# Kernel optimization log

Hardware: AMD Instinct MI355X
Metric: run time of the kernel (lower is better)

## Reference

```python
import jax, jax.numpy as jnp
import numpy as np
from jax import lax

DIM = 512
HEADS = 8


def _branch(x, w1, wd):
    # 1x1 pointwise conv (no bias)
    y = jnp.einsum('oc,bchw->bohw', w1, x)
    # ReflectionPad2d(2)
    y = jnp.pad(y, ((0, 0), (0, 0), (2, 2), (2, 2)), mode='reflect')
    # depthwise 3x3, dilation 2, valid padding (net: same spatial size)
    y = lax.conv_general_dilated(
        y, wd, window_strides=(1, 1), padding='VALID', rhs_dilation=(2, 2),
        dimension_numbers=('NCHW', 'OIHW', 'NCHW'), feature_group_count=y.shape[1])
    return y


def setup_inputs() -> dict:
    key = jax.random.key(0)
    ks = jax.random.split(key, 8)
    s = 0.02
    style_feat = jax.random.normal(ks[0], (16, DIM, 64, 64), dtype=jnp.float32)
    fw1 = jax.random.normal(ks[1], (DIM, DIM), dtype=jnp.float32) * s
    fwd_ = jax.random.normal(ks[2], (DIM, 1, 3, 3), dtype=jnp.float32) * s
    gw1 = jax.random.normal(ks[3], (DIM, DIM), dtype=jnp.float32) * s
    gwd = jax.random.normal(ks[4], (DIM, 1, 3, 3), dtype=jnp.float32) * s
    hw1 = jax.random.normal(ks[5], (DIM, DIM), dtype=jnp.float32) * s
    hwd = jax.random.normal(ks[6], (DIM, 1, 3, 3), dtype=jnp.float32) * s
    ow = jax.random.normal(ks[7], (DIM, DIM), dtype=jnp.float32) * s
    temperature = jnp.ones((HEADS, 1, 1), dtype=jnp.float32)
    return dict(style_feat=style_feat, fw1=fw1, fwd_=fwd_, gw1=gw1, gwd=gwd,
                hw1=hw1, hwd=hwd, ow=ow, temperature=temperature)


def reference(style_feat, fw1, fwd_, gw1, gwd, hw1, hwd, ow, temperature):
    B, C, H, W = style_feat.shape
    cph = C // HEADS
    f_x = _branch(style_feat, fw1, fwd_)
    g_x = _branch(style_feat, gw1, gwd)
    h_x = _branch(style_feat, hw1, hwd)
    q = f_x.reshape(B, HEADS, cph, H * W)
    k = g_x.reshape(B, HEADS, cph, H * W)
    v = h_x.reshape(B, HEADS, cph, H * W)
    # channel-wise attention: [B,h,cph,cph]
    energy = jnp.einsum('bhcn,bhdn->bhcd', q, k)
    attn = jax.nn.softmax(energy * temperature[None], axis=-1)
    out = jnp.einsum('bhcd,bhdn->bhcn', attn, v).reshape(B, C, H, W)
    out = jnp.einsum('oc,bchw->bohw', ow, out)
    return out + style_feat
```

## Files before the change

### kernel.cpp

```cpp
#include <hip/hip_runtime.h>

typedef unsigned short u16;
typedef __bf16 bf8_t __attribute__((ext_vector_type(8)));
typedef short short8 __attribute__((ext_vector_type(8)));
typedef float f32x4 __attribute__((ext_vector_type(4)));

#define DEV __device__ __forceinline__

DEV u16 f2bf(float x) {
  unsigned u = __builtin_bit_cast(unsigned, x);
  return (u16)((u + 0x7FFFu + ((u >> 16) & 1u)) >> 16);
}
DEV float bf2f(u16 x) {
  unsigned u = (unsigned)x << 16;
  return __builtin_bit_cast(float, u);
}

__global__ void k_wconv(const float* __restrict__ f, const float* __restrict__ g,
                        const float* __restrict__ h, u16* __restrict__ out) {
  int i = blockIdx.x * 256 + threadIdx.x;
  float v;
  if (i < 262144) v = f[i];
  else if (i < 524288) v = g[i - 262144];
  else v = h[i - 524288];
  out[i] = f2bf(v);
}

__global__ __launch_bounds__(256) void k_xt(const float* __restrict__ style, u16* __restrict__ Xt) {
  __shared__ float t[32][33];
  int b = blockIdx.z, c0 = blockIdx.y * 32, n0 = blockIdx.x * 32;
  int tid = threadIdx.x, lr = tid >> 5, lc = tid & 31;
  const float* src = style + ((size_t)b * 512 + c0) * 4096 + n0;
#pragma unroll
  for (int it = 0; it < 4; ++it) {
    int r = it * 8 + lr;
    t[r][lc] = src[(size_t)r * 4096 + lc];
  }
  __syncthreads();
  u16* dst = Xt + ((size_t)b * 4096 + n0) * 512 + c0;
#pragma unroll
  for (int it = 0; it < 4; ++it) {
    int n = it * 8 + lr;
    dst[(size_t)n * 512 + lc] = f2bf(t[lc][n]);
  }
}

DEV void gload16(const u16* g, u16* l) {
  __builtin_amdgcn_global_load_lds((__attribute__((address_space(1))) void*)(g),
                                   (__attribute__((address_space(3))) void*)(l), 16, 0, 0);
}

DEV void stage_tile(const u16* __restrict__ src, int row0, int kb,
                    u16* lds, int wave, int lane) {
#pragma unroll
  for (int qq = 0; qq < 2; ++qq) {
    int idx = (wave * 2 + qq) * 64 + lane;
    int r = idx >> 2;
    int cb = (idx & 3) * 8;
    gload16(src + (size_t)(row0 + r) * 512 + (kb + cb),
            lds + (wave * 2 + qq) * 512);
  }
}

__global__ __launch_bounds__(256, 2) void k_gemm_branch(
    const u16* __restrict__ Wbf, const u16* __restrict__ Xt, u16* __restrict__ Y) {
  int z = blockIdx.z;
  int t = z >> 4, b = z & 15;
  const u16* A = Wbf + (size_t)t * (512 * 512);
  const u16* B = Xt + (size_t)b * (4096 * 512);
  u16* C = Y + (size_t)z * (512 * 4096);
  int M0 = blockIdx.y * 128, N0 = blockIdx.x * 128;
  int tid = threadIdx.x, wave = tid >> 6, lane = tid & 63;
  int wm = wave >> 1, wn = wave & 1;
  __shared__ __align__(16) u16 lA[2][128 * 32];
  __shared__ __align__(16) u16 lB[2][128 * 32];
  f32x4 acc[4][4];
#pragma unroll
  for (int m = 0; m < 4; ++m)
#pragma unroll
    for (int n = 0; n < 4; ++n) acc[m][n] = (f32x4){0.f, 0.f, 0.f, 0.f};
  stage_tile(A, M0, 0, &lA[0][0], wave, lane);
  stage_tile(B, N0, 0, &lB[0][0], wave, lane);
  __syncthreads();
  int lrow = lane & 15, lk = (lane >> 4) * 8;
#pragma unroll 2
  for (int kt = 0; kt < 16; ++kt) {
    int cur = kt & 1;
    if (kt < 15) {
      stage_tile(A, M0, (kt + 1) * 32, &lA[cur ^ 1][0], wave, lane);
      stage_tile(B, N0, (kt + 1) * 32, &lB[cur ^ 1][0], wave, lane);
    }
    bf8_t af[4], bff[4];
#pragma unroll
    for (int m = 0; m < 4; ++m)
      af[m] = *(const bf8_t*)&lA[cur][(wm * 64 + m * 16 + lrow) * 32 + lk];
#pragma unroll
    for (int n = 0; n < 4; ++n)
      bff[n] = *(const bf8_t*)&lB[cur][(wn * 64 + n * 16 + lrow) * 32 + lk];
#pragma unroll
    for (int m = 0; m < 4; ++m)
#pragma unroll
      for (int n = 0; n < 4; ++n)
        acc[m][n] = __builtin_amdgcn_mfma_f32_16x16x32_bf16(af[m], bff[n], acc[m][n], 0, 0, 0);
    __syncthreads();
  }
  int orow = (lane >> 4) * 4, ocol = lane & 15;
#pragma unroll
  for (int m = 0; m < 4; ++m)
#pragma unroll
    for (int n = 0; n < 4; ++n) {
      int row = M0 + wm * 64 + m * 16 + orow;
      int col = N0 + wn * 64 + n * 16 + ocol;
      u16* cp = C + (size_t)row * 4096 + col;
#pragma unroll
      for (int i = 0; i < 4; ++i) cp[(size_t)i * 4096] = f2bf(acc[m][n][i]);
    }
}

__global__ __launch_bounds__(256) void k_dw(u16* __restrict__ Y,
    const float* __restrict__ fwd, const float* __restrict__ gwd, const float* __restrict__ hwd) {
  int p = blockIdx.x;
  int c = p & 511;
  int t = p >> 13;
  const float* wsrc = (t == 0) ? fwd : (t == 1) ? gwd : hwd;
  __shared__ float w[9];
  __shared__ float pl[4096];
  int tid = threadIdx.x;
  if (tid < 9) w[tid] = wsrc[c * 9 + tid];
  u16* plane = Y + (size_t)p * 4096;
#pragma unroll
  for (int qq = 0; qq < 2; ++qq) {
    int v = tid * 2 + qq;
    short8 d = *(const short8*)(plane + v * 8);
#pragma unroll
    for (int e = 0; e < 8; ++e) pl[v * 8 + e] = bf2f((u16)d[e]);
  }
  __syncthreads();
  int y = tid >> 2, xb = (tid & 3) * 16;
  float o[16];
#pragma unroll
  for (int e = 0; e < 16; ++e) o[e] = 0.f;
#pragma unroll
  for (int i = 0; i < 3; ++i) {
    int yy = y + 2 * i - 2;
    yy = yy < 0 ? -yy : (yy > 63 ? 126 - yy : yy);
    const float* row = pl + yy * 64;
#pragma unroll
    for (int j = 0; j < 3; ++j) {
      float wv = w[i * 3 + j];
#pragma unroll
      for (int e = 0; e < 16; ++e) {
        int xx = xb + e + 2 * j - 2;
        xx = xx < 0 ? -xx : (xx > 63 ? 126 - xx : xx);
        o[e] += wv * row[xx];
      }
    }
  }
  short8 s0, s1;
#pragma unroll
  for (int e = 0; e < 8; ++e) { s0[e] = (short)f2bf(o[e]); s1[e] = (short)f2bf(o[e + 8]); }
  *(short8*)(plane + y * 64 + xb) = s0;
  *(short8*)(plane + y * 64 + xb + 8) = s1;
}

__global__ __launch_bounds__(256) void k_vt(const u16* __restrict__ Y, u16* __restrict__ Vt) {
  __shared__ u16 tb[64][72];
  int b = blockIdx.z, c0 = blockIdx.y * 64, n0 = blockIdx.x * 64;
  int tid = threadIdx.x, r = tid >> 2, q = tid & 3;
  const u16* src = Y + ((size_t)(32 + b) * 512 + c0) * 4096 + n0;
  short8 d0 = *(const short8*)(src + (size_t)r * 4096 + q * 16);
  short8 d1 = *(const short8*)(src + (size_t)r * 4096 + q * 16 + 8);
#pragma unroll
  for (int e = 0; e < 8; ++e) { tb[r][q * 16 + e] = (u16)d0[e]; tb[r][q * 16 + 8 + e] = (u16)d1[e]; }
  __syncthreads();
  u16* dst = Vt + ((size_t)b * 4096 + n0) * 512 + c0;
  short8 s0, s1;
#pragma unroll
  for (int e = 0; e < 8; ++e) { s0[e] = (short)tb[q * 16 + e][r]; s1[e] = (short)tb[q * 16 + 8 + e][r]; }
  *(short8*)(dst + (size_t)r * 512 + q * 16) = s0;
  *(short8*)(dst + (size_t)r * 512 + q * 16 + 8) = s1;
}

__global__ __launch_bounds__(256) void k_energy(const u16* __restrict__ Y, float* __restrict__ E) {
  int half = blockIdx.x, h = blockIdx.y, b = blockIdx.z;
  int tid = threadIdx.x, wave = tid >> 6, lane = tid & 63;
  const u16* q = Y + ((size_t)b * 512 + h * 64) * 4096;
  const u16* k = Y + ((size_t)(16 + b) * 512 + h * 64) * 4096;
  f32x4 acc[4][4];
#pragma unroll
  for (int m = 0; m < 4; ++m)
#pragma unroll
    for (int n = 0; n < 4; ++n) acc[m][n] = (f32x4){0.f, 0.f, 0.f, 0.f};
  int lrow = lane & 15, lk = (lane >> 4) * 8;
  int nstart = half * 1024 + wave * 256;
#pragma unroll 1
  for (int it = 0; it < 8; ++it) {
    int nb = nstart + it * 32;
    bf8_t af[4], bff[4];
#pragma unroll
    for (int m = 0; m < 4; ++m)
      af[m] = *(const bf8_t*)(q + (size_t)(m * 16 + lrow) * 4096 + nb + lk);
#pragma unroll
    for (int n = 0; n < 4; ++n)
      bff[n] = *(const bf8_t*)(k + (size_t)(n * 16 + lrow) * 4096 + nb + lk);
#pragma unroll
    for (int m = 0; m < 4; ++m)
#pragma unroll
      for (int n = 0; n < 4; ++n)
        acc[m][n] = __builtin_amdgcn_mfma_f32_16x16x32_bf16(af[m], bff[n], acc[m][n], 0, 0, 0);
  }
  __shared__ float red[4][4096];
  int orow = (lane >> 4) * 4, ocol = lane & 15;
#pragma unroll
  for (int m = 0; m < 4; ++m)
#pragma unroll
    for (int n = 0; n < 4; ++n)
#pragma unroll
      for (int i = 0; i < 4; ++i)
        red[wave][(m * 16 + orow + i) * 64 + n * 16 + ocol] = acc[m][n][i];
  __syncthreads();
  float* Eo = E + ((size_t)(half * 16 + b) * 8 + h) * 4096;
  for (int v = tid; v < 4096; v += 256)
    Eo[v] = red[0][v] + red[1][v] + red[2][v] + red[3][v];
}

__global__ __launch_bounds__(64) void k_softmax(float* __restrict__ E, const float* __restrict__ temp) {
  int bh = blockIdx.x;
  int b = bh >> 3, h = bh & 7;
  int c = threadIdx.x;
  float* p0 = E + (((size_t)b * 8 + h) * 64 + c) * 64;
  float tv = temp[h];
  float e[64];
  float mx = -1e30f;
#pragma unroll
  for (int d = 0; d < 64; ++d) {
    float v = (p0[d] + p0[d + 524288] + p0[d + 1048576] + p0[d + 1572864]) * tv;
    e[d] = v;
    mx = fmaxf(mx, v);
  }
  float s = 0.f;
#pragma unroll
  for (int d = 0; d < 64; ++d) { float v = __expf(e[d] - mx); e[d] = v; s += v; }
  float inv = 1.f / s;
#pragma unroll
  for (int d = 0; d < 64; ++d) p0[d] = e[d] * inv;
}

__global__ __launch_bounds__(256) void k_m2(const float* __restrict__ E, const float* __restrict__ ow,
                                            u16* __restrict__ M2) {
  int og = blockIdx.x, h = blockIdx.y, b = blockIdx.z;
  __shared__ float at[4096];
  int tid = threadIdx.x;
  const float* attn = E + ((size_t)b * 8 + h) * 4096;
  for (int v = tid; v < 4096; v += 256) at[v] = attn[v];
  __syncthreads();
  int o = og * 64 + (tid >> 2), dq = (tid & 3) * 16;
  const float* owr = ow + (size_t)o * 512 + h * 64;
  float acc[16];
#pragma unroll
  for (int e = 0; e < 16; ++e) acc[e] = 0.f;
  for (int cc = 0; cc < 64; ++cc) {
    float wv = owr[cc];
#pragma unroll
    for (int e = 0; e < 16; ++e) acc[e] += wv * at[cc * 64 + dq + e];
  }
  u16* dst = M2 + ((size_t)b * 512 + o) * 512 + h * 64 + dq;
  short8 s0, s1;
#pragma unroll
  for (int e = 0; e < 8; ++e) { s0[e] = (short)f2bf(acc[e]); s1[e] = (short)f2bf(acc[e + 8]); }
  *(short8*)dst = s0;
  *(short8*)(dst + 8) = s1;
}

__global__ __launch_bounds__(256, 2) void k_gemm_final(
    const u16* __restrict__ M2, const u16* __restrict__ Vt,
    const float* __restrict__ style, float* __restrict__ out) {
  int b = blockIdx.z;
  const u16* A = M2 + (size_t)b * (512 * 512);
  const u16* B = Vt + (size_t)b * (4096 * 512);
  const float* st = style + (size_t)b * (512 * 4096);
  float* op = out + (size_t)b * (512 * 4096);
  int M0 = blockIdx.y * 128, N0 = blockIdx.x * 128;
  int tid = threadIdx.x, wave = tid >> 6, lane = tid & 63;
  int wm = wave >> 1, wn = wave & 1;
  __shared__ __align__(16) u16 lA[2][128 * 32];
  __shared__ __align__(16) u16 lB[2][128 * 32];
  f32x4 acc[4][4];
#pragma unroll
  for (int m = 0; m < 4; ++m)
#pragma unroll
    for (int n = 0; n < 4; ++n) acc[m][n] = (f32x4){0.f, 0.f, 0.f, 0.f};
  stage_tile(A, M0, 0, &lA[0][0], wave, lane);
  stage_tile(B, N0, 0, &lB[0][0], wave, lane);
  __syncthreads();
  int lrow = lane & 15, lk = (lane >> 4) * 8;
#pragma unroll 2
  for (int kt = 0; kt < 16; ++kt) {
    int cur = kt & 1;
    if (kt < 15) {
      stage_tile(A, M0, (kt + 1) * 32, &lA[cur ^ 1][0], wave, lane);
      stage_tile(B, N0, (kt + 1) * 32, &lB[cur ^ 1][0], wave, lane);
    }
    bf8_t af[4], bff[4];
#pragma unroll
    for (int m = 0; m < 4; ++m)
      af[m] = *(const bf8_t*)&lA[cur][(wm * 64 + m * 16 + lrow) * 32 + lk];
#pragma unroll
    for (int n = 0; n < 4; ++n)
      bff[n] = *(const bf8_t*)&lB[cur][(wn * 64 + n * 16 + lrow) * 32 + lk];
#pragma unroll
    for (int m = 0; m < 4; ++m)
#pragma unroll
      for (int n = 0; n < 4; ++n)
        acc[m][n] = __builtin_amdgcn_mfma_f32_16x16x32_bf16(af[m], bff[n], acc[m][n], 0, 0, 0);
    __syncthreads();
  }
  int orow = (lane >> 4) * 4, ocol = lane & 15;
#pragma unroll
  for (int m = 0; m < 4; ++m)
#pragma unroll
    for (int n = 0; n < 4; ++n) {
      int row = M0 + wm * 64 + m * 16 + orow;
      int col = N0 + wn * 64 + n * 16 + ocol;
      float* cp = op + (size_t)row * 4096 + col;
      const float* sp = st + (size_t)row * 4096 + col;
#pragma unroll
      for (int i = 0; i < 4; ++i) cp[(size_t)i * 4096] = acc[m][n][i] + sp[(size_t)i * 4096];
    }
}


extern "C" void kernel_launch(void* const* d_in, const int* in_sizes, int n_in,
                              void* d_out, int out_size, void* d_ws, size_t ws_size,
                              hipStream_t stream) {
  const float* style = (const float*)d_in[0];
  const float* fw1   = (const float*)d_in[1];
  const float* fwd_  = (const float*)d_in[2];
  const float* gw1   = (const float*)d_in[3];
  const float* gwd   = (const float*)d_in[4];
  const float* hw1   = (const float*)d_in[5];
  const float* hwd   = (const float*)d_in[6];
  const float* ow    = (const float*)d_in[7];
  const float* temp  = (const float*)d_in[8];
  float* out = (float*)d_out;

  char* ws = (char*)d_ws;
  u16*   Wbf = (u16*)(ws + 0);
  u16*   Y   = (u16*)(ws + (size_t)2097152);
  u16*   Xt  = (u16*)(ws + (size_t)203423744);
  u16*   Vt  = Xt;
  float* E   = (float*)(ws + (size_t)270532608);
  u16*   M2  = (u16*)(ws + (size_t)278921216);

  k_wconv<<<3072, 256, 0, stream>>>(fw1, gw1, hw1, Wbf);
  k_xt<<<dim3(128, 16, 16), 256, 0, stream>>>(style, Xt);
  k_gemm_branch<<<dim3(32, 4, 48), 256, 0, stream>>>(Wbf, Xt, Y);
  k_dw<<<24576, 256, 0, stream>>>(Y, fwd_, gwd, hwd);
  k_vt<<<dim3(64, 8, 16), 256, 0, stream>>>(Y, Vt);
  k_energy<<<dim3(4, 8, 16), 256, 0, stream>>>(Y, E);
  k_softmax<<<128, 64, 0, stream>>>(E, temp);
  k_m2<<<dim3(8, 8, 16), 256, 0, stream>>>(E, ow, M2);
  k_gemm_final<<<dim3(32, 4, 16), 256, 0, stream>>>(M2, Vt, style, out);
}
```

Measured before the change: 469.9 us.

## Replace branch GEMM with 256x256 tiled, swizzled, phased MFMA kernel fusing three weights

Replaces the 128x128 branch GEMM with a 512-thread kernel that computes 256x256 tiles over a concatenated 1536-row weight matrix. It uses XOR-swizzled LDS, K-steps of 64, and explicit vmcnt/barrier phasing with setprio around MFMA quads. The Y layout becomes per-batch [1536 rows], and the dw, vt and energy kernels are reindexed to match. The aims are more data reuse per LDS load, fewer bank conflicts, and loads overlapped with math. In exchange it uses more LDS and registers per block, and the hand-scheduled waits add complexity.

```diff
diff --git a/kernel.cpp b/kernel.cpp
--- a/kernel.cpp
+++ b/kernel.cpp
@@ -15,6 +15,16 @@
   unsigned u = (unsigned)x << 16;
   return __builtin_bit_cast(float, u);
 }
+
+DEV void gload16(const u16* g, u16* l) {
+  __builtin_amdgcn_global_load_lds((__attribute__((address_space(1))) void*)(g),
+                                   (__attribute__((address_space(3))) void*)(l), 16, 0, 0);
+}
+
+#define BARRIER() do { asm volatile("" ::: "memory"); __builtin_amdgcn_s_barrier(); asm volatile("" ::: "memory"); } while (0)
+#define VMCNT(n) asm volatile("s_waitcnt vmcnt(" #n ")" ::: "memory")
+#define PRIO1 __builtin_amdgcn_s_setprio(1)
+#define PRIO0 __builtin_amdgcn_s_setprio(0)
 
 __global__ void k_wconv(const float* __restrict__ f, const float* __restrict__ g,
                         const float* __restrict__ h, u16* __restrict__ out) {
@@ -45,9 +55,133 @@
   }
 }
 
-DEV void gload16(const u16* g, u16* l) {
-  __builtin_amdgcn_global_load_lds((__attribute__((address_space(1))) void*)(g),
-                                   (__attribute__((address_space(3))) void*)(l), 16, 0, 0);
+
+DEV void stage_half(const u16* mat, int rc0, int kt, int half,
+                    u16* ldsslot, int wave, int lane) {
+  const u16* base = mat + (size_t)(rc0 + half * 128) * 512 + kt * 64;
+  u16* ldsb = ldsslot + half * (128 * 64);
+#pragma unroll
+  for (int q = 0; q < 2; ++q) {
+    int ci = (wave * 2 + q) * 64 + lane;
+    int r = ci >> 3;
+    int scb = (ci & 7) ^ (r & 7);
+    gload16(base + (size_t)r * 512 + scb * 8, ldsb + (wave * 2 + q) * 512);
+  }
+}
+
+DEV bf8_t rdfrag(const u16* slot, int row, int ks, int lkg) {
+  int off = (ks * 64 + lkg * 16) ^ ((row & 7) << 4);
+  return *(const bf8_t*)((const char*)slot + row * 128 + off);
+}
+
+#define RD_A(dst, slot, mofs)                                     \
+  _Pragma("unroll") for (int m = 0; m < 4; ++m)                   \
+  _Pragma("unroll") for (int ks = 0; ks < 2; ++ks)                \
+    dst[m][ks] = rdfrag(slot, wm * 128 + (mofs) + m * 16 + lrow, ks, lkg);
+
+#define RD_B(dst, slot, nofs)                                     \
+  _Pragma("unroll") for (int n = 0; n < 2; ++n)                   \
+  _Pragma("unroll") for (int ks = 0; ks < 2; ++ks)                \
+    dst[n][ks] = rdfrag(slot, wn * 64 + (nofs) + n * 16 + lrow, ks, lkg);
+
+#define QUAD(AF, BF, MB, NB)                                                              \
+  do {                                                                                    \
+    _Pragma("unroll") for (int m = 0; m < 4; ++m)                                         \
+    _Pragma("unroll") for (int n = 0; n < 2; ++n) {                                       \
+      acc[(MB) + m][(NB) + n] = __builtin_amdgcn_mfma_f32_16x16x32_bf16(                  \
+          AF[m][0], BF[n][0], acc[(MB) + m][(NB) + n], 0, 0, 0);                          \
+      acc[(MB) + m][(NB) + n] = __builtin_amdgcn_mfma_f32_16x16x32_bf16(                  \
+          AF[m][1], BF[n][1], acc[(MB) + m][(NB) + n], 0, 0, 0);                          \
+    }                                                                                     \
+  } while (0)
+
+#define PHASES4(slotA, slotB, S0, S1, S2, S3, VMSTMT)   \
+  RD_A(a0, slotA, 0);                                   \
+  RD_B(b0, slotB, 0);                                   \
+  S0;                                                   \
+  BARRIER();                                            \
+  PRIO1; QUAD(a0, b0, 0, 0); PRIO0;                     \
+  BARRIER();                                            \
+  RD_A(a1, slotA, 64);                                  \
+  S1;                                                   \
+  BARRIER();                                            \
+  PRIO1; QUAD(a1, b0, 4, 0); PRIO0;                     \
+  BARRIER();                                            \
+  RD_B(b1, slotB, 32);                                  \
+  S2;                                                   \
+  BARRIER();                                            \
+  PRIO1; QUAD(a0, b1, 0, 2); PRIO0;                     \
+  BARRIER();                                            \
+  S3;                                                   \
+  BARRIER();                                            \
+  PRIO1; QUAD(a1, b1, 4, 2); PRIO0;                     \
+  VMSTMT;                                               \
+  BARRIER();
+
+__global__ __launch_bounds__(512, 2) void k_gemm256_branch(
+    const u16* __restrict__ Wall, const u16* __restrict__ Xt, u16* __restrict__ Y) {
+  int bid = blockIdx.x;
+  int wg = (bid & 7) * 192 + (bid >> 3);
+  int b = wg / 96;
+  int rr = wg % 96;
+  int nt = rr / 6, mt = rr % 6;
+  int M0 = mt * 256, N0 = nt * 256;
+  const u16* A = Wall;
+  const u16* B = Xt + (size_t)b * (4096 * 512);
+  u16* C = Y + (size_t)b * (1536 * 4096);
+
+  int tid = threadIdx.x, wave = tid >> 6, lane = tid & 63;
+  int wm = wave >> 2, wn = wave & 3;
+  int lrow = lane & 15, lkg = lane >> 4;
+
+  __shared__ __align__(16) u16 lA[2][256 * 64];
+  __shared__ __align__(16) u16 lB[2][256 * 64];
+
+  f32x4 acc[8][4];
+#pragma unroll
+  for (int m = 0; m < 8; ++m)
+#pragma unroll
+    for (int n = 0; n < 4; ++n) acc[m][n] = (f32x4){0.f, 0.f, 0.f, 0.f};
+
+  stage_half(A, M0, 0, 0, lA[0], wave, lane);
+  stage_half(A, M0, 0, 1, lA[0], wave, lane);
+  stage_half(B, N0, 0, 0, lB[0], wave, lane);
+  stage_half(B, N0, 0, 1, lB[0], wave, lane);
+  stage_half(A, M0, 1, 0, lA[1], wave, lane);
+  stage_half(A, M0, 1, 1, lA[1], wave, lane);
+  VMCNT(4);
+  BARRIER();
+
+  bf8_t a0[4][2], a1[4][2], b0[2][2], b1[2][2];
+#pragma unroll 1
+  for (int it = 0; it < 4; ++it) {
+    const int T = it * 2;
+    const bool last = (it == 3);
+    PHASES4(lA[0], lB[0],
+            stage_half(B, N0, T + 1, 0, lB[1], wave, lane),
+            stage_half(B, N0, T + 1, 1, lB[1], wave, lane),
+            if (!last) stage_half(A, M0, T + 2, 0, lA[0], wave, lane),
+            if (!last) stage_half(A, M0, T + 2, 1, lA[0], wave, lane),
+            if (last) { VMCNT(0); } else { VMCNT(4); })
+    PHASES4(lA[1], lB[1],
+            if (!last) stage_half(B, N0, T + 2, 0, lB[0], wave, lane),
+            if (!last) stage_half(B, N0, T + 2, 1, lB[0], wave, lane),
+            if (!last) stage_half(A, M0, T + 3, 0, lA[1], wave, lane),
+            if (!last) stage_half(A, M0, T + 3, 1, lA[1], wave, lane),
+            if (!last) { VMCNT(4); })
+  }
+
+  int orow = lkg * 4, ocol = lrow;
+#pragma unroll
+  for (int am = 0; am < 8; ++am)
+#pragma unroll
+    for (int an = 0; an < 4; ++an) {
+      int row = M0 + wm * 128 + am * 16 + orow;
+      int col = N0 + wn * 64 + an * 16 + ocol;
+      u16* cp = C + (size_t)row * 4096 + col;
+#pragma unroll
+      for (int i = 0; i < 4; ++i) cp[(size_t)i * 4096] = f2bf(acc[am][an][i]);
+    }
 }
 
 DEV void stage_tile(const u16* __restrict__ src, int row0, int kb,
@@ -62,66 +196,11 @@
   }
 }
 
-__global__ __launch_bounds__(256, 2) void k_gemm_branch(
-    const u16* __restrict__ Wbf, const u16* __restrict__ Xt, u16* __restrict__ Y) {
-  int z = blockIdx.z;
-  int t = z >> 4, b = z & 15;
-  const u16* A = Wbf + (size_t)t * (512 * 512);
-  const u16* B = Xt + (size_t)b * (4096 * 512);
-  u16* C = Y + (size_t)z * (512 * 4096);
-  int M0 = blockIdx.y * 128, N0 = blockIdx.x * 128;
-  int tid = threadIdx.x, wave = tid >> 6, lane = tid & 63;
-  int wm = wave >> 1, wn = wave & 1;
-  __shared__ __align__(16) u16 lA[2][128 * 32];
-  __shared__ __align__(16) u16 lB[2][128 * 32];
-  f32x4 acc[4][4];
-#pragma unroll
-  for (int m = 0; m < 4; ++m)
-#pragma unroll
-    for (int n = 0; n < 4; ++n) acc[m][n] = (f32x4){0.f, 0.f, 0.f, 0.f};
-  stage_tile(A, M0, 0, &lA[0][0], wave, lane);
-  stage_tile(B, N0, 0, &lB[0][0], wave, lane);
-  __syncthreads();
-  int lrow = lane & 15, lk = (lane >> 4) * 8;
-#pragma unroll 2
-  for (int kt = 0; kt < 16; ++kt) {
-    int cur = kt & 1;
-    if (kt < 15) {
-      stage_tile(A, M0, (kt + 1) * 32, &lA[cur ^ 1][0], wave, lane);
-      stage_tile(B, N0, (kt + 1) * 32, &lB[cur ^ 1][0], wave, lane);
-    }
-    bf8_t af[4], bff[4];
-#pragma unroll
-    for (int m = 0; m < 4; ++m)
-      af[m] = *(const bf8_t*)&lA[cur][(wm * 64 + m * 16 + lrow) * 32 + lk];
-#pragma unroll
-    for (int n = 0; n < 4; ++n)
-      bff[n] = *(const bf8_t*)&lB[cur][(wn * 64 + n * 16 + lrow) * 32 + lk];
-#pragma unroll
-    for (int m = 0; m < 4; ++m)
-#pragma unroll
-      for (int n = 0; n < 4; ++n)
-        acc[m][n] = __builtin_amdgcn_mfma_f32_16x16x32_bf16(af[m], bff[n], acc[m][n], 0, 0, 0);
-    __syncthreads();
-  }
-  int orow = (lane >> 4) * 4, ocol = lane & 15;
-#pragma unroll
-  for (int m = 0; m < 4; ++m)
-#pragma unroll
-    for (int n = 0; n < 4; ++n) {
-      int row = M0 + wm * 64 + m * 16 + orow;
-      int col = N0 + wn * 64 + n * 16 + ocol;
-      u16* cp = C + (size_t)row * 4096 + col;
-#pragma unroll
-      for (int i = 0; i < 4; ++i) cp[(size_t)i * 4096] = f2bf(acc[m][n][i]);
-    }
-}
-
 __global__ __launch_bounds__(256) void k_dw(u16* __restrict__ Y,
     const float* __restrict__ fwd, const float* __restrict__ gwd, const float* __restrict__ hwd) {
   int p = blockIdx.x;
-  int c = p & 511;
-  int t = p >> 13;
+  int within = p % 1536;
+  int t = within >> 9, c = within & 511;
   const float* wsrc = (t == 0) ? fwd : (t == 1) ? gwd : hwd;
   __shared__ float w[9];
   __shared__ float pl[4096];
@@ -167,7 +246,7 @@
   __shared__ u16 tb[64][72];
   int b = blockIdx.z, c0 = blockIdx.y * 64, n0 = blockIdx.x * 64;
   int tid = threadIdx.x, r = tid >> 2, q = tid & 3;
-  const u16* src = Y + ((size_t)(32 + b) * 512 + c0) * 4096 + n0;
+  const u16* src = Y + ((size_t)b * 1536 + 1024 + c0) * 4096 + n0;
   short8 d0 = *(const short8*)(src + (size_t)r * 4096 + q * 16);
   short8 d1 = *(const short8*)(src + (size_t)r * 4096 + q * 16 + 8);
 #pragma unroll
@@ -184,8 +263,8 @@
 __global__ __launch_bounds__(256) void k_energy(const u16* __restrict__ Y, float* __restrict__ E) {
   int half = blockIdx.x, h = blockIdx.y, b = blockIdx.z;
   int tid = threadIdx.x, wave = tid >> 6, lane = tid & 63;
-  const u16* q = Y + ((size_t)b * 512 + h * 64) * 4096;
-  const u16* k = Y + ((size_t)(16 + b) * 512 + h * 64) * 4096;
+  const u16* q = Y + ((size_t)b * 1536 + h * 64) * 4096;
+  const u16* k = Y + ((size_t)b * 1536 + 512 + h * 64) * 4096;
   f32x4 acc[4][4];
 #pragma unroll
   for (int m = 0; m < 4; ++m)
@@ -354,7 +433,7 @@
 
   k_wconv<<<3072, 256, 0, stream>>>(fw1, gw1, hw1, Wbf);
   k_xt<<<dim3(128, 16, 16), 256, 0, stream>>>(style, Xt);
-  k_gemm_branch<<<dim3(32, 4, 48), 256, 0, stream>>>(Wbf, Xt, Y);
+  k_gemm256_branch<<<1536, 512, 0, stream>>>(Wbf, Xt, Y);
   k_dw<<<24576, 256, 0, stream>>>(Y, fwd_, gwd, hwd);
   k_vt<<<dim3(64, 8, 16), 256, 0, stream>>>(Y, Vt);
   k_energy<<<dim3(4, 8, 16), 256, 0, stream>>>(Y, E);
```

Measured after the change: 478.2 us. About the same (+1.8%).

## Fuse depthwise conv into energy and V-transpose kernels, remap GEMM grid per XCD

Applied to the files above, without the earlier changes.

The branch GEMM now treats the three pointwise weights as one 1536-row matrix and uses a flat grid that assigns two batches to each XCD, so each batch's Xt stays in that XCD's L2. The separate depthwise-conv, V-transpose and energy kernels are replaced by two fused kernels. k_dwE computes the dilated 3x3 conv for q and k into swizzled LDS and feeds MFMA energy accumulation over row bands. k_dwV convolves v and writes it transposed straight to Vt. This removes an in-place rewrite of Y and a separate transpose pass over global memory, at the cost of recomputing reflection indexing in registers and lower parallelism in the fused kernels.

```diff
diff --git a/kernel.cpp b/kernel.cpp
--- a/kernel.cpp
+++ b/kernel.cpp
@@ -14,6 +14,11 @@
 DEV float bf2f(u16 x) {
   unsigned u = (unsigned)x << 16;
   return __builtin_bit_cast(float, u);
+}
+
+DEV void gload16(const u16* g, u16* l) {
+  __builtin_amdgcn_global_load_lds((__attribute__((address_space(1))) void*)(g),
+                                   (__attribute__((address_space(3))) void*)(l), 16, 0, 0);
 }
 
 __global__ void k_wconv(const float* __restrict__ f, const float* __restrict__ g,
@@ -45,11 +50,6 @@
   }
 }
 
-DEV void gload16(const u16* g, u16* l) {
-  __builtin_amdgcn_global_load_lds((__attribute__((address_space(1))) void*)(g),
-                                   (__attribute__((address_space(3))) void*)(l), 16, 0, 0);
-}
-
 DEV void stage_tile(const u16* __restrict__ src, int row0, int kb,
                     u16* lds, int wave, int lane) {
 #pragma unroll
@@ -63,13 +63,17 @@
 }
 
 __global__ __launch_bounds__(256, 2) void k_gemm_branch(
-    const u16* __restrict__ Wbf, const u16* __restrict__ Xt, u16* __restrict__ Y) {
-  int z = blockIdx.z;
-  int t = z >> 4, b = z & 15;
-  const u16* A = Wbf + (size_t)t * (512 * 512);
+    const u16* __restrict__ Wall, const u16* __restrict__ Xt, u16* __restrict__ Y) {
+  int bid = blockIdx.x;
+  int xcd = bid & 7, idx = bid >> 3;
+  int bh = idx / 384;
+  int r = idx - bh * 384;
+  int b = xcd * 2 + bh;
+  int nt = r / 12, mt = r - nt * 12;
+  int M0 = mt * 128, N0 = nt * 128;
+  const u16* A = Wall;
   const u16* B = Xt + (size_t)b * (4096 * 512);
-  u16* C = Y + (size_t)z * (512 * 4096);
-  int M0 = blockIdx.y * 128, N0 = blockIdx.x * 128;
+  u16* C = Y + (size_t)b * (1536 * 4096);
   int tid = threadIdx.x, wave = tid >> 6, lane = tid & 63;
   int wm = wave >> 1, wn = wave & 1;
   __shared__ __align__(16) u16 lA[2][128 * 32];
@@ -117,111 +121,146 @@
     }
 }
 
-__global__ __launch_bounds__(256) void k_dw(u16* __restrict__ Y,
-    const float* __restrict__ fwd, const float* __restrict__ gwd, const float* __restrict__ hwd) {
-  int p = blockIdx.x;
-  int c = p & 511;
-  int t = p >> 13;
-  const float* wsrc = (t == 0) ? fwd : (t == 1) ? gwd : hwd;
-  __shared__ float w[9];
-  __shared__ float pl[4096];
-  int tid = threadIdx.x;
-  if (tid < 9) w[tid] = wsrc[c * 9 + tid];
-  u16* plane = Y + (size_t)p * 4096;
-#pragma unroll
-  for (int qq = 0; qq < 2; ++qq) {
-    int v = tid * 2 + qq;
-    short8 d = *(const short8*)(plane + v * 8);
-#pragma unroll
-    for (int e = 0; e < 8; ++e) pl[v * 8 + e] = bf2f((u16)d[e]);
-  }
-  __syncthreads();
-  int y = tid >> 2, xb = (tid & 3) * 16;
-  float o[16];
-#pragma unroll
-  for (int e = 0; e < 16; ++e) o[e] = 0.f;
+template <typename F>
+DEV void dw_row(const u16* plane, const float* w9, int y, F&& store) {
+  short8 raw[3][8];
 #pragma unroll
   for (int i = 0; i < 3; ++i) {
     int yy = y + 2 * i - 2;
     yy = yy < 0 ? -yy : (yy > 63 ? 126 - yy : yy);
-    const float* row = pl + yy * 64;
-#pragma unroll
-    for (int j = 0; j < 3; ++j) {
-      float wv = w[i * 3 + j];
-#pragma unroll
-      for (int e = 0; e < 16; ++e) {
-        int xx = xb + e + 2 * j - 2;
-        xx = xx < 0 ? -xx : (xx > 63 ? 126 - xx : xx);
-        o[e] += wv * row[xx];
+    const short8* rp = (const short8*)(plane + yy * 64);
+#pragma unroll
+    for (int ch = 0; ch < 8; ++ch) raw[i][ch] = rp[ch];
+  }
+#pragma unroll
+  for (int g = 0; g < 4; ++g) {
+    float fr[3][20];
+#pragma unroll
+    for (int t = 0; t < 20; ++t) {
+      int p = g * 16 - 2 + t;
+      int rp2 = p < 0 ? -p : (p > 63 ? 126 - p : p);
+#pragma unroll
+      for (int i = 0; i < 3; ++i)
+        fr[i][t] = bf2f((u16)raw[i][rp2 >> 3][rp2 & 7]);
+    }
+    float o[16];
+#pragma unroll
+    for (int e = 0; e < 16; ++e) {
+      float s = 0.f;
+#pragma unroll
+      for (int i = 0; i < 3; ++i)
+#pragma unroll
+        for (int j = 0; j < 3; ++j)
+          s += w9[i * 3 + j] * fr[i][e + 2 * j];
+      o[e] = s;
+    }
+    store(g, o);
+  }
+}
+
+__global__ __launch_bounds__(256, 2) void k_dwE(const u16* __restrict__ Y,
+    const float* __restrict__ fwd, const float* __restrict__ gwd, float* __restrict__ E) {
+  int band = blockIdx.x, h = blockIdx.y, b = blockIdx.z;
+  __shared__ __align__(16) u16 qbuf[64 * 256];
+  __shared__ __align__(16) u16 kbuf[64 * 256];
+  int tid = threadIdx.x;
+  int c = ((tid >> 5) << 3) | (tid & 7);
+  int yl = (tid >> 3) & 3;
+  int wv = tid >> 6, lane = tid & 63;
+  int lrow = lane & 15, lkg = lane >> 4;
+  const u16* qp = Y + ((size_t)b * 1536 + h * 64 + c) * 4096;
+  const u16* kp = Y + ((size_t)b * 1536 + 512 + h * 64 + c) * 4096;
+  float wq9[9], wk9[9];
+#pragma unroll
+  for (int t = 0; t < 9; ++t) {
+    wq9[t] = fwd[(h * 64 + c) * 9 + t];
+    wk9[t] = gwd[(h * 64 + c) * 9 + t];
+  }
+  f32x4 acc[4];
+#pragma unroll
+  for (int n = 0; n < 4; ++n) acc[n] = (f32x4){0.f, 0.f, 0.f, 0.f};
+  char* qrow = (char*)qbuf + c * 512;
+  char* krow = (char*)kbuf + c * 512;
+  int c7 = c & 7;
+#pragma unroll 1
+  for (int sb = 0; sb < 4; ++sb) {
+    int y = band * 16 + sb * 4 + yl;
+    dw_row(qp, wq9, y, [&](int g, const float* o) {
+      short8 s0, s1;
+#pragma unroll
+      for (int e = 0; e < 8; ++e) { s0[e] = (short)f2bf(o[e]); s1[e] = (short)f2bf(o[e + 8]); }
+      int ch0 = yl * 8 + g * 2;
+      *(short8*)(qrow + 16 * (ch0 ^ c7)) = s0;
+      *(short8*)(qrow + 16 * ((ch0 + 1) ^ c7)) = s1;
+    });
+    dw_row(kp, wk9, y, [&](int g, const float* o) {
+      short8 s0, s1;
+#pragma unroll
+      for (int e = 0; e < 8; ++e) { s0[e] = (short)f2bf(o[e]); s1[e] = (short)f2bf(o[e + 8]); }
+      int ch0 = yl * 8 + g * 2;
+      *(short8*)(krow + 16 * (ch0 ^ c7)) = s0;
+      *(short8*)(krow + 16 * ((ch0 + 1) ^ c7)) = s1;
+    });
+    __syncthreads();
+    const char* qb = (const char*)qbuf + (wv * 16 + lrow) * 512;
+    int ca7 = (wv * 16 + lrow) & 7;
+#pragma unroll
+    for (int ks = 0; ks < 8; ++ks) {
+      bf8_t aF = *(const bf8_t*)(qb + 16 * ((ks * 4 + lkg) ^ ca7));
+#pragma unroll
+      for (int n = 0; n < 4; ++n) {
+        int cb = n * 16 + lrow;
+        bf8_t bF = *(const bf8_t*)((const char*)kbuf + cb * 512 + 16 * ((ks * 4 + lkg) ^ (cb & 7)));
+        acc[n] = __builtin_amdgcn_mfma_f32_16x16x32_bf16(aF, bF, acc[n], 0, 0, 0);
       }
     }
-  }
-  short8 s0, s1;
-#pragma unroll
-  for (int e = 0; e < 8; ++e) { s0[e] = (short)f2bf(o[e]); s1[e] = (short)f2bf(o[e + 8]); }
-  *(short8*)(plane + y * 64 + xb) = s0;
-  *(short8*)(plane + y * 64 + xb + 8) = s1;
-}
-
-__global__ __launch_bounds__(256) void k_vt(const u16* __restrict__ Y, u16* __restrict__ Vt) {
-  __shared__ u16 tb[64][72];
-  int b = blockIdx.z, c0 = blockIdx.y * 64, n0 = blockIdx.x * 64;
-  int tid = threadIdx.x, r = tid >> 2, q = tid & 3;
-  const u16* src = Y + ((size_t)(32 + b) * 512 + c0) * 4096 + n0;
-  short8 d0 = *(const short8*)(src + (size_t)r * 4096 + q * 16);
-  short8 d1 = *(const short8*)(src + (size_t)r * 4096 + q * 16 + 8);
-#pragma unroll
-  for (int e = 0; e < 8; ++e) { tb[r][q * 16 + e] = (u16)d0[e]; tb[r][q * 16 + 8 + e] = (u16)d1[e]; }
-  __syncthreads();
-  u16* dst = Vt + ((size_t)b * 4096 + n0) * 512 + c0;
-  short8 s0, s1;
-#pragma unroll
-  for (int e = 0; e < 8; ++e) { s0[e] = (short)tb[q * 16 + e][r]; s1[e] = (short)tb[q * 16 + 8 + e][r]; }
-  *(short8*)(dst + (size_t)r * 512 + q * 16) = s0;
-  *(short8*)(dst + (size_t)r * 512 + q * 16 + 8) = s1;
-}
-
-__global__ __launch_bounds__(256) void k_energy(const u16* __restrict__ Y, float* __restrict__ E) {
-  int half = blockIdx.x, h = blockIdx.y, b = blockIdx.z;
-  int tid = threadIdx.x, wave = tid >> 6, lane = tid & 63;
-  const u16* q = Y + ((size_t)b * 512 + h * 64) * 4096;
-  const u16* k = Y + ((size_t)(16 + b) * 512 + h * 64) * 4096;
-  f32x4 acc[4][4];
-#pragma unroll
-  for (int m = 0; m < 4; ++m)
-#pragma unroll
-    for (int n = 0; n < 4; ++n) acc[m][n] = (f32x4){0.f, 0.f, 0.f, 0.f};
-  int lrow = lane & 15, lk = (lane >> 4) * 8;
-  int nstart = half * 1024 + wave * 256;
+    __syncthreads();
+  }
+  float* Eo = E + (((size_t)band * 16 + b) * 8 + h) * 4096;
+  int orow = (lane >> 4) * 4, ocol = lane & 15;
+#pragma unroll
+  for (int n = 0; n < 4; ++n)
+#pragma unroll
+    for (int i = 0; i < 4; ++i)
+      Eo[(wv * 16 + orow + i) * 64 + n * 16 + ocol] = acc[n][i];
+}
+
+__global__ __launch_bounds__(256, 2) void k_dwV(const u16* __restrict__ Y,
+    const float* __restrict__ hwd, u16* __restrict__ Vt) {
+  int band = blockIdx.x, ct = blockIdx.y, b = blockIdx.z;
+  __shared__ float vb[256 * 68];
+  int tid = threadIdx.x;
+  int c = ((tid >> 5) << 3) | (tid & 7);
+  int yl = (tid >> 3) & 3;
+  int cg = tid & 7;
+  int cglob = ct * 64 + c;
+  const u16* plane = Y + ((size_t)b * 1536 + 1024 + cglob) * 4096;
+  float w9[9];
+#pragma unroll
+  for (int t = 0; t < 9; ++t) w9[t] = hwd[cglob * 9 + t];
 #pragma unroll 1
-  for (int it = 0; it < 8; ++it) {
-    int nb = nstart + it * 32;
-    bf8_t af[4], bff[4];
-#pragma unroll
-    for (int m = 0; m < 4; ++m)
-      af[m] = *(const bf8_t*)(q + (size_t)(m * 16 + lrow) * 4096 + nb + lk);
-#pragma unroll
-    for (int n = 0; n < 4; ++n)
-      bff[n] = *(const bf8_t*)(k + (size_t)(n * 16 + lrow) * 4096 + nb + lk);
-#pragma unroll
-    for (int m = 0; m < 4; ++m)
-#pragma unroll
-      for (int n = 0; n < 4; ++n)
-        acc[m][n] = __builtin_amdgcn_mfma_f32_16x16x32_bf16(af[m], bff[n], acc[m][n], 0, 0, 0);
-  }
-  __shared__ float red[4][4096];
-  int orow = (lane >> 4) * 4, ocol = lane & 15;
-#pragma unroll
-  for (int m = 0; m < 4; ++m)
-#pragma unroll
-    for (int n = 0; n < 4; ++n)
-#pragma unroll
-      for (int i = 0; i < 4; ++i)
-        red[wave][(m * 16 + orow + i) * 64 + n * 16 + ocol] = acc[m][n][i];
-  __syncthreads();
-  float* Eo = E + ((size_t)(half * 16 + b) * 8 + h) * 4096;
-  for (int v = tid; v < 4096; v += 256)
-    Eo[v] = red[0][v] + red[1][v] + red[2][v] + red[3][v];
+  for (int sb = 0; sb < 4; ++sb) {
+    int y = band * 16 + sb * 4 + yl;
+    dw_row(plane, w9, y, [&](int g, const float* o) {
+#pragma unroll
+      for (int e = 0; e < 16; ++e)
+        vb[((g * 16 + e) * 4 + yl) * 68 + c] = o[e];
+    });
+    __syncthreads();
+#pragma unroll
+    for (int k = 0; k < 8; ++k) {
+      int np = (tid >> 3) + 32 * k;
+      int x = np >> 2, yy = np & 3;
+      int ng = (band * 16 + sb * 4 + yy) * 64 + x;
+      f32x4 r0 = *(const f32x4*)&vb[np * 68 + cg * 8];
+      f32x4 r1 = *(const f32x4*)&vb[np * 68 + cg * 8 + 4];
+      short8 s;
+#pragma unroll
+      for (int e = 0; e < 4; ++e) { s[e] = (short)f2bf(r0[e]); s[e + 4] = (short)f2bf(r1[e]); }
+      *(short8*)(Vt + ((size_t)b * 4096 + ng) * 512 + ct * 64 + cg * 8) = s;
+    }
+    __syncthreads();
+  }
 }
 
 __global__ __launch_bounds__(64) void k_softmax(float* __restrict__ E, const float* __restrict__ temp) {
@@ -354,10 +393,9 @@
 
   k_wconv<<<3072, 256, 0, stream>>>(fw1, gw1, hw1, Wbf);
   k_xt<<<dim3(128, 16, 16), 256, 0, stream>>>(style, Xt);
-  k_gemm_branch<<<dim3(32, 4, 48), 256, 0, stream>>>(Wbf, Xt, Y);
-  k_dw<<<24576, 256, 0, stream>>>(Y, fwd_, gwd, hwd);
-  k_vt<<<dim3(64, 8, 16), 256, 0, stream>>>(Y, Vt);
-  k_energy<<<dim3(4, 8, 16), 256, 0, stream>>>(Y, E);
+  k_gemm_branch<<<6144, 256, 0, stream>>>(Wbf, Xt, Y);
+  k_dwE<<<dim3(4, 8, 16), 256, 0, stream>>>(Y, fwd_, gwd, E);
+  k_dwV<<<dim3(4, 8, 16), 256, 0, stream>>>(Y, hwd, Vt);
   k_softmax<<<128, 64, 0, stream>>>(E, temp);
   k_m2<<<dim3(8, 8, 16), 256, 0, stream>>>(E, ow, M2);
   k_gemm_final<<<dim3(32, 4, 16), 256, 0, stream>>>(M2, Vt, style, out);
```

After: 408.4 us. 1.15x faster.
